# Kernel tuning notes

Measured on AMD Instinct MI355X. Metric: run time of the kernel, lower is better.

## Reference

```python
import jax, jax.numpy as jnp
import numpy as np


def setup_inputs() -> dict:
    key = jax.random.key(0)
    k0, k1, k2 = jax.random.split(key, 3)
    B, N, C = 2, 2048, 1024
    x = jax.random.normal(k0, (B, N, C), jnp.float32)
    W_qkv = jax.random.normal(k1, (3 * C, C), jnp.float32) * 0.02
    b_qkv = jnp.zeros((3 * C,), jnp.float32)
    W_out = jax.random.normal(k2, (C, C), jnp.float32) * 0.02
    b_out = jnp.zeros((C,), jnp.float32)
    return {"x": x, "W_qkv": W_qkv, "b_qkv": b_qkv, "W_out": W_out, "b_out": b_out, "n_heads": 16}


def reference(x, W_qkv, b_qkv, W_out, b_out, n_heads):
    B, N, C = x.shape
    dk = C // n_heads
    scale = 1.0 / np.sqrt(dk)
    # qkv projection -> (3, B, H, N, dk)
    qkv = (x @ W_qkv.T + b_qkv).reshape(B, N, 3, n_heads, dk).transpose(2, 0, 3, 1, 4)
    q, k, v = qkv[0], qkv[1], qkv[2]
    attn_all = jnp.einsum('bhqd,bhkd->bhqk', q, k) * scale  # (B,H,N,N)
    # sparsity measure per query row: max - mean
    M = jnp.max(attn_all, axis=-1) - jnp.mean(attn_all, axis=-1)  # (B,H,N)
    n_top = max(1, min(int(N * 0.25), N - 1))
    _, top_idx = jax.lax.top_k(M, n_top)  # (B,H,n_top)
    # keep[b,h,q] = True iff query row q is among top rows (vectorized scatter,
    # replaces the original per-(b,h) python loop)
    b_idx = jnp.arange(B)[:, None, None]
    h_idx = jnp.arange(n_heads)[None, :, None]
    keep = jnp.zeros((B, n_heads, N), bool).at[b_idx, h_idx, top_idx].set(True)
    # non-top query rows are fully masked to -1e9 (as in masked_fill)
    attn = jnp.where(keep[..., None], attn_all, jnp.float32(-1e9))
    attn = jax.nn.softmax(attn, axis=-1)
    # dropout is identity in eval mode
    out = jnp.einsum('bhqk,bhkd->bhqd', attn, v)
    out = out.transpose(0, 2, 1, 3).reshape(B, N, C)
    return out @ W_out.T + b_out
```

## Files before the change

kernel.cpp:

```cpp
#include <hip/hip_runtime.h>
#include <math.h>

typedef unsigned short u16;
typedef __attribute__((ext_vector_type(8))) short short8v;
typedef __attribute__((ext_vector_type(4))) float f32x4;

constexpr int B  = 2;
constexpr int N  = 2048;
constexpr int C  = 1024;
constexpr int H  = 16;
constexpr int DK = 64;
constexpr int NTOP = 512;
constexpr float SCALE = 0.125f;
constexpr int   BAND_CAP = 1024;
constexpr float BAND_EPS = 2e-3f;
constexpr int   CSEG = 16;

__device__ __forceinline__ void gload16(const u16* g, u16* l) {
    __builtin_amdgcn_global_load_lds(
        (const __attribute__((address_space(1))) unsigned int*)g,
        (__attribute__((address_space(3))) unsigned int*)l,
        16, 0, 0);
}

__device__ __forceinline__ u16 bf16_rne(float x) {
    unsigned u = __float_as_uint(x);
    unsigned r = u + 0x7fffu + ((u >> 16) & 1u);
    return (u16)(r >> 16);
}

__global__ __launch_bounds__(256) void convert_hilo(
    const float* __restrict__ src, u16* __restrict__ hi, u16* __restrict__ lo, int n)
{
    int i = (blockIdx.x * 256 + threadIdx.x) * 4;
    if (i >= n) return;
    float4 v = *(const float4*)&src[i];
    u16 h0 = bf16_rne(v.x), h1 = bf16_rne(v.y), h2 = bf16_rne(v.z), h3 = bf16_rne(v.w);
    float f0 = __uint_as_float((unsigned)h0 << 16);
    float f1 = __uint_as_float((unsigned)h1 << 16);
    float f2 = __uint_as_float((unsigned)h2 << 16);
    float f3 = __uint_as_float((unsigned)h3 << 16);
    *(ushort4*)&hi[i] = make_ushort4(h0, h1, h2, h3);
    *(ushort4*)&lo[i] = make_ushort4(bf16_rne(v.x - f0), bf16_rne(v.y - f1),
                                     bf16_rne(v.z - f2), bf16_rne(v.w - f3));
}

__global__ __launch_bounds__(256) void convert_hilo_T(
    const float* __restrict__ v, u16* __restrict__ th, u16* __restrict__ tl)
{
    constexpr int LS = 68;
    __shared__ u16 Sh[64 * LS], Sl[64 * LS];
    const int bh = blockIdx.y;
    const int kt = blockIdx.x * 64;
    const int tid = threadIdx.x;
    #pragma unroll
    for (int p = 0; p < 4; ++p) {
        int idx = tid * 4 + p * 1024;
        int key = idx >> 6, d = idx & 63;
        float4 x4 = *(const float4*)&v[((size_t)bh * N + kt + key) * DK + d];
        float xs[4] = {x4.x, x4.y, x4.z, x4.w};
        ushort4 hh, ll;
        u16* hp = (u16*)&hh; u16* lp = (u16*)&ll;
        #pragma unroll
        for (int j = 0; j < 4; ++j) {
            u16 h = bf16_rne(xs[j]);
            hp[j] = h;
            lp[j] = bf16_rne(xs[j] - __uint_as_float((unsigned)h << 16));
        }
        *(ushort4*)&Sh[key * LS + d] = hh;
        *(ushort4*)&Sl[key * LS + d] = ll;
    }
    __syncthreads();
    const int d = tid >> 2, seg = tid & 3;
    u16 bufh[16], bufl[16];
    #pragma unroll
    for (int i = 0; i < 16; ++i) {
        bufh[i] = Sh[(seg * 16 + i) * LS + d];
        bufl[i] = Sl[(seg * 16 + i) * LS + d];
    }
    size_t oa = ((size_t)bh * DK + d) * N + kt + seg * 16;
    *(uint4*)&th[oa] = ((uint4*)bufh)[0];
    *(uint4*)&th[oa + 8] = ((uint4*)bufh)[1];
    *(uint4*)&tl[oa] = ((uint4*)bufl)[0];
    *(uint4*)&tl[oa + 8] = ((uint4*)bufl)[1];
}

template <int MODE>
__global__ __launch_bounds__(256) void gemm_mfma(
    const u16* __restrict__ Ahi, const u16* __restrict__ Alo,
    const u16* __restrict__ Bhi, const u16* __restrict__ Blo,
    const float* __restrict__ bias, float* __restrict__ out,
    float* __restrict__ qb, float* __restrict__ kb, float* __restrict__ vb,
    int K)
{
    __shared__ __align__(16) u16 Ah[128 * 32], Al[128 * 32];
    __shared__ __align__(16) u16 Bh[128 * 32], Bl[128 * 32];

    const int tid = threadIdx.x;
    const int m0 = blockIdx.y * 128;
    const int n0 = blockIdx.x * 128;
    const int lane = tid & 63;
    const int wave = tid >> 6;
    const int wr = wave >> 1, wc = wave & 1;
    const int fr = lane & 15, sl = lane >> 4;

    const u16* gsrc = (wave == 0) ? Ahi + (size_t)m0 * K
                    : (wave == 1) ? Alo + (size_t)m0 * K
                    : (wave == 2) ? Bhi + (size_t)n0 * K
                                  : Blo + (size_t)n0 * K;
    u16* lbase = (wave == 0) ? Ah : (wave == 1) ? Al : (wave == 2) ? Bh : Bl;

    f32x4 acc[4][4] = {};

    for (int k0 = 0; k0 < K; k0 += 32) {
        __syncthreads();
        #pragma unroll
        for (int i = 0; i < 8; ++i) {
            int c = i * 64 + lane;
            int row = c >> 2, sp = c & 3;
            int gs = sp ^ ((row >> 1) & 3);
            gload16(gsrc + (size_t)row * K + k0 + gs * 8, lbase + i * 512);
        }
        __syncthreads();

        short8v afh[4], afl[4], bfh[4], bfl[4];
        #pragma unroll
        for (int m = 0; m < 4; ++m) {
            int row = wr * 64 + m * 16 + fr;
            int off = row * 32 + ((sl ^ ((row >> 1) & 3)) * 8);
            afh[m] = *(const short8v*)&Ah[off];
            afl[m] = *(const short8v*)&Al[off];
        }
        #pragma unroll
        for (int n = 0; n < 4; ++n) {
            int row = wc * 64 + n * 16 + fr;
            int off = row * 32 + ((sl ^ ((row >> 1) & 3)) * 8);
            bfh[n] = *(const short8v*)&Bh[off];
            bfl[n] = *(const short8v*)&Bl[off];
        }
        #pragma unroll
        for (int m = 0; m < 4; ++m)
            #pragma unroll
            for (int n = 0; n < 4; ++n) {
                acc[m][n] = __builtin_amdgcn_mfma_f32_16x16x32_bf16(afh[m], bfh[n], acc[m][n], 0, 0, 0);
                acc[m][n] = __builtin_amdgcn_mfma_f32_16x16x32_bf16(afh[m], bfl[n], acc[m][n], 0, 0, 0);
                acc[m][n] = __builtin_amdgcn_mfma_f32_16x16x32_bf16(afl[m], bfh[n], acc[m][n], 0, 0, 0);
            }
    }

    #pragma unroll
    for (int m = 0; m < 4; ++m)
        #pragma unroll
        for (int n = 0; n < 4; ++n)
            #pragma unroll
            for (int r = 0; r < 4; ++r) {
                int grow = m0 + wr * 64 + m * 16 + sl * 4 + r;
                int gcol = n0 + wc * 64 + n * 16 + fr;
                float val = acc[m][n][r] + bias[gcol];
                if (MODE == 0) {
                    int t = gcol >> 10, h = (gcol >> 6) & 15, d = gcol & 63;
                    int bb = grow >> 11, nn = grow & (N - 1);
                    float* dst = (t == 0) ? qb : (t == 1) ? kb : vb;
                    dst[(((size_t)bb * H + h) * N + nn) * DK + d] = val;
                } else {
                    out[(size_t)grow * C + gcol] = val;
                }
            }
}

__global__ __launch_bounds__(256) void colsum_part(
    const float* __restrict__ src, float* __restrict__ partial)
{
    const int bh = blockIdx.y, seg = blockIdx.x;
    const int d = threadIdx.x & 63;
    const int sub = threadIdx.x >> 6;
    const int k0 = seg * (N / CSEG);
    float s = 0.f;
    for (int kk = sub; kk < N / CSEG; kk += 4)
        s += src[((size_t)bh * N + k0 + kk) * DK + d];
    __shared__ float part[4][64];
    part[sub][d] = s;
    __syncthreads();
    if (threadIdx.x < 64)
        partial[((size_t)bh * CSEG + seg) * DK + d] =
            part[0][d] + part[1][d] + part[2][d] + part[3][d];
}

__global__ __launch_bounds__(64) void colsum_final(
    const float* __restrict__ partial, float* __restrict__ mean)
{
    const int bh = blockIdx.x, d = threadIdx.x;
    float s = 0.f;
    #pragma unroll
    for (int g = 0; g < CSEG; ++g) s += partial[((size_t)bh * CSEG + g) * DK + d];
    mean[bh * DK + d] = s / (float)N;
}

__global__ __launch_bounds__(256) void qdot_kernel(
    const float* __restrict__ q, const float* __restrict__ kmean,
    float* __restrict__ Mdot)
{
    const int bh = blockIdx.y;
    const int row = blockIdx.x * 256 + threadIdx.x;
    __shared__ float km[DK];
    if (threadIdx.x < DK) km[threadIdx.x] = kmean[bh * DK + threadIdx.x];
    __syncthreads();
    const float* qr = &q[((size_t)bh * N + row) * DK];
    float s = 0.f;
    #pragma unroll
    for (int d4 = 0; d4 < DK; d4 += 4) {
        float4 v = *(const float4*)&qr[d4];
        s += v.x * km[d4] + v.y * km[d4 + 1] + v.z * km[d4 + 2] + v.w * km[d4 + 3];
    }
    Mdot[(size_t)bh * N + row] = s;
}

__global__ __launch_bounds__(256) void row_stats_mfma(
    const u16* __restrict__ qh_, const u16* __restrict__ ql_,
    const u16* __restrict__ kh_, const u16* __restrict__ kl_,
    const float* __restrict__ Mdot, float* __restrict__ Mout,
    float* __restrict__ rowmax)
{
    __shared__ __align__(16) u16 Kh[64 * 64];
    __shared__ __align__(16) u16 Kl[64 * 64];
    const int tid = threadIdx.x, lane = tid & 63, wave = tid >> 6;
    const int bh = blockIdx.y;
    const int q0 = blockIdx.x * 128 + wave * 32;
    const int fr = lane & 15, g = lane >> 4;

    const u16* gsrc = (wave & 2) ? kl_ : kh_;
    u16* lbase = (wave & 2) ? Kl : Kh;
    const int cb = (wave & 1) * 256;

    short8v qfh[2][2], qfl[2][2];
    #pragma unroll
    for (int m = 0; m < 2; ++m)
        #pragma unroll
        for (int kk = 0; kk < 2; ++kk) {
            size_t qa = ((size_t)bh * N + q0 + m * 16 + fr) * DK + kk * 32 + g * 8;
            qfh[m][kk] = *(const short8v*)&qh_[qa];
            qfl[m][kk] = *(const short8v*)&ql_[qa];
        }

    f32x4 mx[2];
    mx[0] = (f32x4){-1e30f, -1e30f, -1e30f, -1e30f};
    mx[1] = mx[0];

    for (int kt = 0; kt < N; kt += 64) {
        __syncthreads();
        #pragma unroll
        for (int i = 0; i < 4; ++i) {
            int c = cb + i * 64 + lane;
            int row = c >> 3, sp = c & 7;
            int gs = sp ^ (row & 7);
            gload16(gsrc + ((size_t)bh * N + kt + row) * DK + gs * 8,
                    lbase + (size_t)(cb + i * 64) * 8);
        }
        __syncthreads();
        short8v bfh[4][2], bfl[4][2];
        #pragma unroll
        for (int n = 0; n < 4; ++n)
            #pragma unroll
            for (int kk = 0; kk < 2; ++kk) {
                int key = n * 16 + fr;
                int off = key * 64 + (((g + kk * 4) ^ (key & 7)) * 8);
                bfh[n][kk] = *(const short8v*)&Kh[off];
                bfl[n][kk] = *(const short8v*)&Kl[off];
            }
        #pragma unroll
        for (int m = 0; m < 2; ++m)
            #pragma unroll
            for (int n = 0; n < 4; ++n) {
                f32x4 a = {};
                #pragma unroll
                for (int kk = 0; kk < 2; ++kk) {
                    a = __builtin_amdgcn_mfma_f32_16x16x32_bf16(qfl[m][kk], bfh[n][kk], a, 0, 0, 0);
                    a = __builtin_amdgcn_mfma_f32_16x16x32_bf16(qfh[m][kk], bfl[n][kk], a, 0, 0, 0);
                    a = __builtin_amdgcn_mfma_f32_16x16x32_bf16(qfh[m][kk], bfh[n][kk], a, 0, 0, 0);
                }
                #pragma unroll
                for (int r = 0; r < 4; ++r) mx[m][r] = fmaxf(mx[m][r], a[r]);
            }
    }

    #pragma unroll
    for (int w = 1; w < 16; w <<= 1)
        #pragma unroll
        for (int m = 0; m < 2; ++m)
            #pragma unroll
            for (int r = 0; r < 4; ++r)
                mx[m][r] = fmaxf(mx[m][r], __shfl_xor(mx[m][r], w, 64));

    if (fr == 0) {
        #pragma unroll
        for (int m = 0; m < 2; ++m)
            #pragma unroll
            for (int r = 0; r < 4; ++r) {
                int row = q0 + m * 16 + g * 4 + r;
                size_t idx = (size_t)bh * N + row;
                float v = mx[m][r];
                rowmax[idx] = SCALE * v;
                Mout[idx]   = SCALE * (v - Mdot[idx]);
            }
    }
}

__global__ void zero_cnt(int* cnt) { if (threadIdx.x < B * H) cnt[threadIdx.x] = 0; }

__global__ __launch_bounds__(256) void topk_thr(
    const float* __restrict__ Mv, float* __restrict__ thr)
{
    const int bh = blockIdx.y;
    const int qi = blockIdx.x * 256 + threadIdx.x;
    __shared__ float Ms[N];
    for (int e = threadIdx.x; e < N; e += 256) Ms[e] = Mv[(size_t)bh * N + e];
    __syncthreads();
    const float mq = Ms[qi];
    int rank = 0;
    for (int j = 0; j < N; ++j) {
        float mj = Ms[j];
        rank += (mj > mq) || (mj == mq && j < qi);
    }
    if (rank == NTOP - 1) thr[bh] = mq;
}

__global__ __launch_bounds__(256) void band_classify(
    const float* __restrict__ Mv, const float* __restrict__ thr,
    int* __restrict__ cnt, int* __restrict__ band, int* __restrict__ keep)
{
    const int bh = blockIdx.y;
    const int row = blockIdx.x * 256 + threadIdx.x;
    const float m = Mv[(size_t)bh * N + row];
    const float t = thr[bh];
    int kp;
    if (fabsf(m - t) <= BAND_EPS) {
        int pos = atomicAdd(&cnt[bh], 1);
        if (pos < BAND_CAP) band[bh * BAND_CAP + pos] = row;
        kp = 0;
    } else {
        kp = (m > t) ? 1 : 0;
    }
    keep[(size_t)bh * N + row] = kp;
}

__global__ __launch_bounds__(256) void refine_kernel(
    const float* __restrict__ q, const float* __restrict__ k,
    const int* __restrict__ cnt, const int* __restrict__ band,
    float* __restrict__ Mv)
{
    constexpr int LS = 69;
    __shared__ float Ks[64 * LS];
    __shared__ float qs[DK];
    const int bh = blockIdx.y;
    const int tid = threadIdx.x;
    const int n = min(cnt[bh], BAND_CAP);
    for (int ci = blockIdx.x; ci < n; ci += 32) {
        const int row = band[bh * BAND_CAP + ci];
        __syncthreads();
        if (tid < DK) qs[tid] = q[((size_t)bh * N + row) * DK + tid];
        double mx = -1e30, sm = 0.0;
        for (int kt = 0; kt < N; kt += 64) {
            __syncthreads();
            #pragma unroll
            for (int p = 0; p < 4; ++p) {
                int idx = tid * 4 + p * 1024;
                int kr = idx >> 6, d = idx & 63;
                float4 x4 = *(const float4*)&k[((size_t)bh * N + kt + kr) * DK + d];
                Ks[kr * LS + d]     = x4.x;
                Ks[kr * LS + d + 1] = x4.y;
                Ks[kr * LS + d + 2] = x4.z;
                Ks[kr * LS + d + 3] = x4.w;
            }
            __syncthreads();
            if (tid < 64) {
                double s = 0.0;
                #pragma unroll
                for (int d = 0; d < DK; ++d)
                    s += (double)qs[d] * (double)Ks[tid * LS + d];
                mx = fmax(mx, s);
                sm += s;
            }
        }
        if (tid < 64) {
            #pragma unroll
            for (int w = 1; w < 64; w <<= 1) {
                mx = fmax(mx, __shfl_xor(mx, w, 64));
                sm += __shfl_xor(sm, w, 64);
            }
            if (tid == 0)
                Mv[(size_t)bh * N + row] = (float)((double)SCALE * (mx - sm / (double)N));
        }
    }
}

__global__ __launch_bounds__(256) void band_finalize(
    const float* __restrict__ Mv, const int* __restrict__ cnt,
    const int* __restrict__ band, int* __restrict__ keep,
    int* __restrict__ kidx)
{
    __shared__ unsigned char kL[N];
    __shared__ int   bRow[BAND_CAP];
    __shared__ float bM[BAND_CAP];
    __shared__ int aW[4];
    __shared__ int scan[256];

    const int bh = blockIdx.x;
    const int tid = threadIdx.x;
    const int lane = tid & 63, wid = tid >> 6;
    const int nb = min(cnt[bh], BAND_CAP);

    int above = 0;
    #pragma unroll
    for (int w = 0; w < 8; ++w) {
        int row = w * 256 + tid;
        int kp = keep[(size_t)bh * N + row];
        kL[row] = (unsigned char)kp;
        above += kp;
    }
    #pragma unroll
    for (int w = 1; w < 64; w <<= 1) above += __shfl_xor(above, w, 64);
    if (lane == 0) aW[wid] = above;
    for (int i = tid; i < nb; i += 256) {
        int r = band[bh * BAND_CAP + i];
        bRow[i] = r;
        bM[i] = Mv[(size_t)bh * N + r];
    }
    __syncthreads();
    const int nAbove = aW[0] + aW[1] + aW[2] + aW[3];

    for (int i = tid; i < nb; i += 256) {
        const float mi = bM[i];
        const int ri = bRow[i];
        int rank = nAbove;
        for (int j = 0; j < nb; ++j) {
            float mj = bM[j];
            rank += (mj > mi) || (mj == mi && bRow[j] < ri);
        }
        int kp = (rank < NTOP) ? 1 : 0;
        kL[ri] = (unsigned char)kp;
        keep[(size_t)bh * N + ri] = kp;
    }
    __syncthreads();

    int cntL = 0;
    #pragma unroll
    for (int r = 0; r < 8; ++r) cntL += kL[tid * 8 + r];
    scan[tid] = cntL;
    __syncthreads();
    for (int s = 1; s < 256; s <<= 1) {
        int v = (tid >= s) ? scan[tid - s] : 0;
        __syncthreads();
        scan[tid] += v;
        __syncthreads();
    }
    int pos = scan[tid] - cntL;
    #pragma unroll
    for (int r = 0; r < 8; ++r) {
        int row = tid * 8 + r;
        if (kL[row]) kidx[bh * NTOP + pos++] = row;
    }
}

__global__ __launch_bounds__(256) void fill_nonkept(
    const int* __restrict__ keep, const float* __restrict__ vmean,
    float* __restrict__ attn_out)
{
    const int bh = blockIdx.y;
    const int b = bh >> 4, h = bh & 15;
    const int d = threadIdx.x & 63;
    const int rr = threadIdx.x >> 6;
    const float vm = vmean[bh * DK + d];
    #pragma unroll
    for (int i = 0; i < 16; ++i) {
        int row = blockIdx.x * 64 + i * 4 + rr;
        if (!keep[(size_t)bh * N + row])
            attn_out[((size_t)b * N + row) * C + h * DK + d] = vm;
    }
}

__global__ __launch_bounds__(256) void attn_mfma(
    const u16* __restrict__ qh_, const u16* __restrict__ ql_,
    const u16* __restrict__ kh_, const u16* __restrict__ kl_,
    const u16* __restrict__ vth_, const u16* __restrict__ vtl_,
    const float* __restrict__ rowmax, const int* __restrict__ kidx,
    float* __restrict__ attn_out)
{
    __shared__ __align__(16) u16 Kh[64 * 64], Kl[64 * 64];
    __shared__ __align__(16) u16 Vh[64 * 64], Vl[64 * 64];
    __shared__ __align__(16) u16 Ph[4][16 * 64], Pl[4][16 * 64];

    const int tid = threadIdx.x, lane = tid & 63, wave = tid >> 6;
    const int wg = blockIdx.x;
    const int bh = ((wg >> 6) << 3) | (wg & 7);
    const int xblk = (wg >> 3) & 7;
    const int b = bh >> 4, h = bh & 15;
    const int q0 = xblk * 64 + wave * 16;
    const int fr = lane & 15, sl = lane >> 4;

    const bool isV = (wave >= 2);
    const u16* ksrc = (wave & 1) ? kl_ : kh_;
    const u16* vsrc = (wave & 1) ? vtl_ : vth_;
    u16* lbase = (wave == 0) ? Kh : (wave == 1) ? Kl : (wave == 2) ? Vh : Vl;
    const size_t kbase0 = (size_t)bh * N * DK;
    const size_t vbase0 = (size_t)bh * DK * N;

    const int* kix = kidx + bh * NTOP;
    const int qrow_f = kix[q0 + fr];
    int qr_o[4]; float rmax_r[4];
    #pragma unroll
    for (int r = 0; r < 4; ++r) {
        qr_o[r] = kix[q0 + sl * 4 + r];
        rmax_r[r] = rowmax[(size_t)bh * N + qr_o[r]];
    }

    short8v qfh[2], qfl[2];
    #pragma unroll
    for (int kk = 0; kk < 2; ++kk) {
        size_t qa = ((size_t)bh * N + qrow_f) * DK + kk * 32 + sl * 8;
        qfh[kk] = *(const short8v*)&qh_[qa];
        qfl[kk] = *(const short8v*)&ql_[qa];
    }

    f32x4 opv[4] = {};
    float lsum[4] = {};

    for (int kt = 0; kt < N; kt += 64) {
        __syncthreads();
        #pragma unroll
        for (int i = 0; i < 8; ++i) {
            int c = i * 64 + lane;
            int row = c >> 3, sp = c & 7;
            int gs = sp ^ (row & 7);
            const u16* g = isV ? (vsrc + vbase0 + (size_t)row * N + kt + gs * 8)
                               : (ksrc + kbase0 + (size_t)(kt + row) * DK + gs * 8);
            gload16(g, lbase + (size_t)i * 512);
        }
        __syncthreads();

        #pragma unroll
        for (int n = 0; n < 4; ++n) {
            f32x4 a = {};
            #pragma unroll
            for (int kk = 0; kk < 2; ++kk) {
                int key = n * 16 + fr;
                int off = key * 64 + (((sl + kk * 4) ^ (key & 7)) * 8);
                short8v bh_f = *(const short8v*)&Kh[off];
                short8v bl_f = *(const short8v*)&Kl[off];
                a = __builtin_amdgcn_mfma_f32_16x16x32_bf16(qfl[kk], bh_f, a, 0, 0, 0);
                a = __builtin_amdgcn_mfma_f32_16x16x32_bf16(qfh[kk], bl_f, a, 0, 0, 0);
                a = __builtin_amdgcn_mfma_f32_16x16x32_bf16(qfh[kk], bh_f, a, 0, 0, 0);
            }
            #pragma unroll
            for (int r = 0; r < 4; ++r) {
                float p = __expf(a[r] * SCALE - rmax_r[r]);
                lsum[r] += p;
                u16 ph = bf16_rne(p);
                u16 pl = bf16_rne(p - __uint_as_float((unsigned)ph << 16));
                int q_l = sl * 4 + r;
                int key = n * 16 + fr;
                int off = q_l * 64 + (((key >> 3) ^ (q_l & 7)) * 8) + (key & 7);
                Ph[wave][off] = ph;
                Pl[wave][off] = pl;
            }
        }

        #pragma unroll
        for (int kk = 0; kk < 2; ++kk) {
            int aoff = fr * 64 + (((kk * 4 + sl) ^ (fr & 7)) * 8);
            short8v pah = *(const short8v*)&Ph[wave][aoff];
            short8v pal = *(const short8v*)&Pl[wave][aoff];
            #pragma unroll
            for (int n = 0; n < 4; ++n) {
                int d = n * 16 + fr;
                int voff = d * 64 + (((kk * 4 + sl) ^ (d & 7)) * 8);
                short8v vhf = *(const short8v*)&Vh[voff];
                short8v vlf = *(const short8v*)&Vl[voff];
                opv[n] = __builtin_amdgcn_mfma_f32_16x16x32_bf16(pal, vhf, opv[n], 0, 0, 0);
                opv[n] = __builtin_amdgcn_mfma_f32_16x16x32_bf16(pah, vlf, opv[n], 0, 0, 0);
                opv[n] = __builtin_amdgcn_mfma_f32_16x16x32_bf16(pah, vhf, opv[n], 0, 0, 0);
            }
        }
    }

    #pragma unroll
    for (int w = 1; w < 16; w <<= 1)
        #pragma unroll
        for (int r = 0; r < 4; ++r)
            lsum[r] += __shfl_xor(lsum[r], w, 64);

    #pragma unroll
    for (int r = 0; r < 4; ++r) {
        const float inv = 1.0f / lsum[r];
        float* orow = attn_out + ((size_t)b * N + qr_o[r]) * C + h * DK;
        #pragma unroll
        for (int n = 0; n < 4; ++n)
            orow[n * 16 + fr] = opv[n][r] * inv;
    }
}

extern "C" void kernel_launch(void* const* d_in, const int* in_sizes, int n_in,
                              void* d_out, int out_size, void* d_ws, size_t ws_size,
                              hipStream_t stream)
{
    const float* x    = (const float*)d_in[0];
    const float* Wqkv = (const float*)d_in[1];
    const float* bqkv = (const float*)d_in[2];
    const float* Wout = (const float*)d_in[3];
    const float* bout = (const float*)d_in[4];
    float* out = (float*)d_out;

    char* ws = (char*)d_ws;
    size_t off = 0;
    auto alloc = [&](size_t bytes) -> void* {
        void* p = ws + off;
        off += (bytes + 255) & ~(size_t)255;
        return p;
    };

    const size_t BHND = (size_t)B * H * N * DK;
    float* q        = (float*)alloc(BHND * 4);
    float* kbuf     = (float*)alloc(BHND * 4);
    float* vbuf     = (float*)alloc(BHND * 4);
    float* attn_out = (float*)alloc((size_t)B * N * C * 4);
    u16* cvAhi = (u16*)alloc((size_t)B * N * C * 2);
    u16* cvAlo = (u16*)alloc((size_t)B * N * C * 2);
    u16* cvBhi = (u16*)alloc((size_t)3 * C * C * 2);
    u16* cvBlo = (u16*)alloc((size_t)3 * C * C * 2);
    u16* qhi   = (u16*)alloc(BHND * 2);
    u16* qlo   = (u16*)alloc(BHND * 2);
    u16* khi   = (u16*)alloc(BHND * 2);
    u16* klo   = (u16*)alloc(BHND * 2);
    u16* vthi  = (u16*)alloc(BHND * 2);
    u16* vtlo  = (u16*)alloc(BHND * 2);
    float* Mbuf     = (float*)alloc((size_t)B * H * N * 4);
    float* rmaxbuf  = (float*)alloc((size_t)B * H * N * 4);
    float* Mdot     = (float*)alloc((size_t)B * H * N * 4);
    int*   keep     = (int*)  alloc((size_t)B * H * N * 4);
    int*   kidx     = (int*)  alloc((size_t)B * H * NTOP * 4);
    float* vmeanbuf = (float*)alloc((size_t)B * H * DK * 4);
    float* kmeanbuf = (float*)alloc((size_t)B * H * DK * 4);
    float* partbuf  = (float*)alloc((size_t)B * H * CSEG * DK * 4);
    float* thrbuf   = (float*)alloc((size_t)B * H * 4);
    int*   cntbuf   = (int*)  alloc((size_t)B * H * 4);
    int*   bandbuf  = (int*)  alloc((size_t)B * H * BAND_CAP * 4);

    const int nX = B * N * C;
    const int nW = 3 * C * C;
    const int nWo = C * C;

    convert_hilo<<<nX / 1024, 256, 0, stream>>>(x, cvAhi, cvAlo, nX);
    convert_hilo<<<nW / 1024, 256, 0, stream>>>(Wqkv, cvBhi, cvBlo, nW);

    gemm_mfma<0><<<dim3(3 * C / 128, (B * N) / 128), 256, 0, stream>>>(
        cvAhi, cvAlo, cvBhi, cvBlo, bqkv, nullptr, q, kbuf, vbuf, C);

    convert_hilo<<<nX / 1024, 256, 0, stream>>>(q, qhi, qlo, nX);
    convert_hilo<<<nX / 1024, 256, 0, stream>>>(kbuf, khi, klo, nX);
    convert_hilo_T<<<dim3(N / 64, B * H), 256, 0, stream>>>(vbuf, vthi, vtlo);

    colsum_part<<<dim3(CSEG, B * H), 256, 0, stream>>>(vbuf, partbuf);
    colsum_final<<<B * H, 64, 0, stream>>>(partbuf, vmeanbuf);
    colsum_part<<<dim3(CSEG, B * H), 256, 0, stream>>>(kbuf, partbuf);
    colsum_final<<<B * H, 64, 0, stream>>>(partbuf, kmeanbuf);

    qdot_kernel<<<dim3(N / 256, B * H), 256, 0, stream>>>(q, kmeanbuf, Mdot);

    row_stats_mfma<<<dim3(N / 128, B * H), 256, 0, stream>>>(
        qhi, qlo, khi, klo, Mdot, Mbuf, rmaxbuf);

    zero_cnt<<<1, 64, 0, stream>>>(cntbuf);
    topk_thr<<<dim3(N / 256, B * H), 256, 0, stream>>>(Mbuf, thrbuf);
    band_classify<<<dim3(N / 256, B * H), 256, 0, stream>>>(Mbuf, thrbuf, cntbuf, bandbuf, keep);
    refine_kernel<<<dim3(32, B * H), 256, 0, stream>>>(q, kbuf, cntbuf, bandbuf, Mbuf);
    band_finalize<<<B * H, 256, 0, stream>>>(Mbuf, cntbuf, bandbuf, keep, kidx);

    fill_nonkept<<<dim3(N / 64, B * H), 256, 0, stream>>>(keep, vmeanbuf, attn_out);
    attn_mfma<<<256, 256, 0, stream>>>(
        qhi, qlo, khi, klo, vthi, vtlo, rmaxbuf, kidx, attn_out);

    convert_hilo<<<nX / 1024, 256, 0, stream>>>(attn_out, cvAhi, cvAlo, nX);
    convert_hilo<<<nWo / 1024, 256, 0, stream>>>(Wout, cvBhi, cvBlo, nWo);
    gemm_mfma<1><<<dim3(C / 128, (B * N) / 128), 256, 0, stream>>>(
        cvAhi, cvAlo, cvBhi, cvBlo, bout, out, nullptr, nullptr, nullptr, C);
}
```

Measured before the change: 417.3 us.

## Merge small launches, add XCD-aware block swizzle, and set MFMA wave priority

Merges the q/k hi-lo conversions into one launch, the two colsum passes into one part and one final kernel, and folds the count zeroing into topk_thr, which cuts launch overhead. The GEMM and row_stats kernels now use a 1D grid with a swizzle that assigns consecutive tiles to the same XCD (bid&7), aiming for better L2 reuse. The attention kernel raises wave priority around its MFMA sections. The swizzle assumes the grid size is divisible by 8, and cnt is zeroed by one block inside topk_thr, which is safe only because band_classify is a later launch on the same stream.

Result: faster. 405.7 us (-2.8%).

```diff
diff --git a/kernel.cpp b/kernel.cpp
--- a/kernel.cpp
+++ b/kernel.cpp
@@ -45,6 +45,27 @@
                                      bf16_rne(v.z - f2), bf16_rne(v.w - f3));
 }
 
+__global__ __launch_bounds__(256) void convert_hilo2(
+    const float* __restrict__ a, const float* __restrict__ b,
+    u16* __restrict__ ah, u16* __restrict__ al,
+    u16* __restrict__ bh_, u16* __restrict__ bl_, int n)
+{
+    const float* src = blockIdx.y ? b : a;
+    u16* hi = blockIdx.y ? bh_ : ah;
+    u16* lo = blockIdx.y ? bl_ : al;
+    int i = (blockIdx.x * 256 + threadIdx.x) * 4;
+    if (i >= n) return;
+    float4 v = *(const float4*)&src[i];
+    u16 h0 = bf16_rne(v.x), h1 = bf16_rne(v.y), h2 = bf16_rne(v.z), h3 = bf16_rne(v.w);
+    float f0 = __uint_as_float((unsigned)h0 << 16);
+    float f1 = __uint_as_float((unsigned)h1 << 16);
+    float f2 = __uint_as_float((unsigned)h2 << 16);
+    float f3 = __uint_as_float((unsigned)h3 << 16);
+    *(ushort4*)&hi[i] = make_ushort4(h0, h1, h2, h3);
+    *(ushort4*)&lo[i] = make_ushort4(bf16_rne(v.x - f0), bf16_rne(v.y - f1),
+                                     bf16_rne(v.z - f2), bf16_rne(v.w - f3));
+}
+
 __global__ __launch_bounds__(256) void convert_hilo_T(
     const float* __restrict__ v, u16* __restrict__ th, u16* __restrict__ tl)
 {
@@ -91,14 +112,19 @@
     const u16* __restrict__ Bhi, const u16* __restrict__ Blo,
     const float* __restrict__ bias, float* __restrict__ out,
     float* __restrict__ qb, float* __restrict__ kb, float* __restrict__ vb,
-    int K)
+    int K, int ntx)
 {
     __shared__ __align__(16) u16 Ah[128 * 32], Al[128 * 32];
     __shared__ __align__(16) u16 Bh[128 * 32], Bl[128 * 32];
 
+    const int nwg = gridDim.x;
+    const int cpx = nwg >> 3;
+    const int bid = blockIdx.x;
+    const int swz = (bid & 7) * cpx + (bid >> 3);
+    const int m0 = (swz / ntx) * 128;
+    const int n0 = (swz % ntx) * 128;
+
     const int tid = threadIdx.x;
-    const int m0 = blockIdx.y * 128;
-    const int n0 = blockIdx.x * 128;
     const int lane = tid & 63;
     const int wave = tid >> 6;
     const int wr = wave >> 1, wc = wave & 1;
@@ -168,10 +194,12 @@
             }
 }
 
-__global__ __launch_bounds__(256) void colsum_part(
-    const float* __restrict__ src, float* __restrict__ partial)
-{
-    const int bh = blockIdx.y, seg = blockIdx.x;
+__global__ __launch_bounds__(256) void colsum_part2(
+    const float* __restrict__ v, const float* __restrict__ k,
+    float* __restrict__ partial)
+{
+    const int bh = blockIdx.y, seg = blockIdx.x, which = blockIdx.z;
+    const float* src = which ? k : v;
     const int d = threadIdx.x & 63;
     const int sub = threadIdx.x >> 6;
     const int k0 = seg * (N / CSEG);
@@ -182,18 +210,23 @@
     part[sub][d] = s;
     __syncthreads();
     if (threadIdx.x < 64)
-        partial[((size_t)bh * CSEG + seg) * DK + d] =
+        partial[(((size_t)which * B * H + bh) * CSEG + seg) * DK + d] =
             part[0][d] + part[1][d] + part[2][d] + part[3][d];
 }
 
-__global__ __launch_bounds__(64) void colsum_final(
-    const float* __restrict__ partial, float* __restrict__ mean)
-{
-    const int bh = blockIdx.x, d = threadIdx.x;
+__global__ __launch_bounds__(128) void colsum_final2(
+    const float* __restrict__ partial, float* __restrict__ vmean,
+    float* __restrict__ kmean)
+{
+    const int bh = blockIdx.x;
+    const int d = threadIdx.x & 63;
+    const int which = threadIdx.x >> 6;
+    const float* p = partial + ((size_t)which * B * H + bh) * CSEG * DK;
     float s = 0.f;
     #pragma unroll
-    for (int g = 0; g < CSEG; ++g) s += partial[((size_t)bh * CSEG + g) * DK + d];
-    mean[bh * DK + d] = s / (float)N;
+    for (int g = 0; g < CSEG; ++g) s += p[g * DK + d];
+    float* dst = which ? kmean : vmean;
+    dst[bh * DK + d] = s / (float)N;
 }
 
 __global__ __launch_bounds__(256) void qdot_kernel(
@@ -224,8 +257,13 @@
     __shared__ __align__(16) u16 Kh[64 * 64];
     __shared__ __align__(16) u16 Kl[64 * 64];
     const int tid = threadIdx.x, lane = tid & 63, wave = tid >> 6;
-    const int bh = blockIdx.y;
-    const int q0 = blockIdx.x * 128 + wave * 32;
+
+    const int nwg = gridDim.x;
+    const int cpx = nwg >> 3;
+    const int bid = blockIdx.x;
+    const int swz = (bid & 7) * cpx + (bid >> 3);
+    const int bh = swz >> 4;
+    const int q0 = (swz & 15) * 128 + wave * 32;
     const int fr = lane & 15, g = lane >> 4;
 
     const u16* gsrc = (wave & 2) ? kl_ : kh_;
@@ -305,13 +343,12 @@
     }
 }
 
-__global__ void zero_cnt(int* cnt) { if (threadIdx.x < B * H) cnt[threadIdx.x] = 0; }
-
 __global__ __launch_bounds__(256) void topk_thr(
-    const float* __restrict__ Mv, float* __restrict__ thr)
+    const float* __restrict__ Mv, float* __restrict__ thr, int* __restrict__ cnt)
 {
     const int bh = blockIdx.y;
     const int qi = blockIdx.x * 256 + threadIdx.x;
+    if (blockIdx.x == 0 && threadIdx.x == 0) cnt[bh] = 0;
     __shared__ float Ms[N];
     for (int e = threadIdx.x; e < N; e += 256) Ms[e] = Mv[(size_t)bh * N + e];
     __syncthreads();
@@ -540,6 +577,7 @@
         #pragma unroll
         for (int n = 0; n < 4; ++n) {
             f32x4 a = {};
+            __builtin_amdgcn_s_setprio(1);
             #pragma unroll
             for (int kk = 0; kk < 2; ++kk) {
                 int key = n * 16 + fr;
@@ -550,6 +588,7 @@
                 a = __builtin_amdgcn_mfma_f32_16x16x32_bf16(qfh[kk], bl_f, a, 0, 0, 0);
                 a = __builtin_amdgcn_mfma_f32_16x16x32_bf16(qfh[kk], bh_f, a, 0, 0, 0);
             }
+            __builtin_amdgcn_s_setprio(0);
             #pragma unroll
             for (int r = 0; r < 4; ++r) {
                 float p = __expf(a[r] * SCALE - rmax_r[r]);
@@ -564,6 +603,7 @@
             }
         }
 
+        __builtin_amdgcn_s_setprio(1);
         #pragma unroll
         for (int kk = 0; kk < 2; ++kk) {
             int aoff = fr * 64 + (((kk * 4 + sl) ^ (fr & 7)) * 8);
@@ -580,6 +620,7 @@
                 opv[n] = __builtin_amdgcn_mfma_f32_16x16x32_bf16(pah, vhf, opv[n], 0, 0, 0);
             }
         }
+        __builtin_amdgcn_s_setprio(0);
     }
 
     #pragma unroll
@@ -639,7 +680,7 @@
     int*   kidx     = (int*)  alloc((size_t)B * H * NTOP * 4);
     float* vmeanbuf = (float*)alloc((size_t)B * H * DK * 4);
     float* kmeanbuf = (float*)alloc((size_t)B * H * DK * 4);
-    float* partbuf  = (float*)alloc((size_t)B * H * CSEG * DK * 4);
+    float* partbuf  = (float*)alloc((size_t)2 * B * H * CSEG * DK * 4);
     float* thrbuf   = (float*)alloc((size_t)B * H * 4);
     int*   cntbuf   = (int*)  alloc((size_t)B * H * 4);
     int*   bandbuf  = (int*)  alloc((size_t)B * H * BAND_CAP * 4);
@@ -651,25 +692,22 @@
     convert_hilo<<<nX / 1024, 256, 0, stream>>>(x, cvAhi, cvAlo, nX);
     convert_hilo<<<nW / 1024, 256, 0, stream>>>(Wqkv, cvBhi, cvBlo, nW);
 
-    gemm_mfma<0><<<dim3(3 * C / 128, (B * N) / 128), 256, 0, stream>>>(
-        cvAhi, cvAlo, cvBhi, cvBlo, bqkv, nullptr, q, kbuf, vbuf, C);
-
-    convert_hilo<<<nX / 1024, 256, 0, stream>>>(q, qhi, qlo, nX);
-    convert_hilo<<<nX / 1024, 256, 0, stream>>>(kbuf, khi, klo, nX);
+    gemm_mfma<0><<<768, 256, 0, stream>>>(
+        cvAhi, cvAlo, cvBhi, cvBlo, bqkv, nullptr, q, kbuf, vbuf, C, 24);
+
+    convert_hilo2<<<dim3(nX / 1024, 2), 256, 0, stream>>>(
+        q, kbuf, qhi, qlo, khi, klo, nX);
     convert_hilo_T<<<dim3(N / 64, B * H), 256, 0, stream>>>(vbuf, vthi, vtlo);
 
-    colsum_part<<<dim3(CSEG, B * H), 256, 0, stream>>>(vbuf, partbuf);
-    colsum_final<<<B * H, 64, 0, stream>>>(partbuf, vmeanbuf);
-    colsum_part<<<dim3(CSEG, B * H), 256, 0, stream>>>(kbuf, partbuf);
-    colsum_final<<<B * H, 64, 0, stream>>>(partbuf, kmeanbuf);
+    colsum_part2<<<dim3(CSEG, B * H, 2), 256, 0, stream>>>(vbuf, kbuf, partbuf);
+    colsum_final2<<<B * H, 128, 0, stream>>>(partbuf, vmeanbuf, kmeanbuf);
 
     qdot_kernel<<<dim3(N / 256, B * H), 256, 0, stream>>>(q, kmeanbuf, Mdot);
 
-    row_stats_mfma<<<dim3(N / 128, B * H), 256, 0, stream>>>(
+    row_stats_mfma<<<512, 256, 0, stream>>>(
         qhi, qlo, khi, klo, Mdot, Mbuf, rmaxbuf);
 
-    zero_cnt<<<1, 64, 0, stream>>>(cntbuf);
-    topk_thr<<<dim3(N / 256, B * H), 256, 0, stream>>>(Mbuf, thrbuf);
+    topk_thr<<<dim3(N / 256, B * H), 256, 0, stream>>>(Mbuf, thrbuf, cntbuf);
     band_classify<<<dim3(N / 256, B * H), 256, 0, stream>>>(Mbuf, thrbuf, cntbuf, bandbuf, keep);
     refine_kernel<<<dim3(32, B * H), 256, 0, stream>>>(q, kbuf, cntbuf, bandbuf, Mbuf);
     band_finalize<<<B * H, 256, 0, stream>>>(Mbuf, cntbuf, bandbuf, keep, kidx);
@@ -680,6 +718,6 @@
 
     convert_hilo<<<nX / 1024, 256, 0, stream>>>(attn_out, cvAhi, cvAlo, nX);
     convert_hilo<<<nWo / 1024, 256, 0, stream>>>(Wout, cvBhi, cvBlo, nWo);
-    gemm_mfma<1><<<dim3(C / 128, (B * N) / 128), 256, 0, stream>>>(
-        cvAhi, cvAlo, cvBhi, cvBlo, bout, out, nullptr, nullptr, nullptr, C);
-}
+    gemm_mfma<1><<<256, 256, 0, stream>>>(
+        cvAhi, cvAlo, cvBhi, cvBlo, bout, out, nullptr, nullptr, nullptr, C, 8);
+}
```
